# Kernel tuning notes

Measured on AMD Instinct MI355X. Metric: run time of the kernel, lower is better.

The kernel has to match this reference:

```python
import jax, jax.numpy as jnp
import numpy as np

N, E = 50000, 800000          # nodes, edges (avg degree 16)
D_IN, D_H, D_OUT = 128, 128, 64
BN_EPS = 1e-5


def setup_inputs() -> dict:
    key = jax.random.key(0)
    ks = jax.random.split(key, 8)
    g = lambda k, shp, s: jax.random.normal(k, shp, jnp.float32) * s
    return {
        "x": jax.random.normal(ks[0], (N, D_IN), jnp.float32),
        "edge_index": jax.random.randint(ks[1], (2, E), 0, N),
        # SAGEConv layer 1: lin_l (neighbors, with bias), lin_r (root, no bias)
        "Wl1": g(ks[2], (D_IN, D_H), 0.05),
        "Wr1": g(ks[3], (D_IN, D_H), 0.05),
        "b1": jnp.zeros((D_H,), jnp.float32),
        # BatchNorm1d(hidden)
        "gamma": jnp.ones((D_H,), jnp.float32),
        "beta": jnp.zeros((D_H,), jnp.float32),
        # SAGEConv layer 2
        "Wl2": g(ks[4], (D_H, D_OUT), 0.05),
        "Wr2": g(ks[5], (D_H, D_OUT), 0.05),
        "b2": jnp.zeros((D_OUT,), jnp.float32),
    }


def _sage_conv(x, src, dst, Wl, Wr, b):
    """PyG SAGEConv (mean aggr): lin_l(mean_{j in N(i)} x_j) + lin_r(x_i)."""
    n = x.shape[0]
    agg = jax.ops.segment_sum(x[src], dst, num_segments=n)            # [N, d]
    cnt = jax.ops.segment_sum(jnp.ones((src.shape[0],), x.dtype), dst,
                              num_segments=n)                          # [N]
    agg = agg / jnp.maximum(cnt, 1.0)[:, None]                         # mean, 0 for isolated
    return agg @ Wl + x @ Wr + b


def _batch_norm(x, gamma, beta):
    """Training-mode BatchNorm1d: batch stats over the node axis, biased var."""
    mu = jnp.mean(x, axis=0)
    var = jnp.var(x, axis=0)
    return gamma * (x - mu) * jax.lax.rsqrt(var + BN_EPS) + beta


def reference(x, edge_index, Wl1, Wr1, b1, gamma, beta, Wl2, Wr2, b2):
    src, dst = edge_index[0], edge_index[1]
    h = _sage_conv(x, src, dst, Wl1, Wr1, b1)
    h = jax.nn.relu(_batch_norm(h, gamma, beta))
    # dropout is identity in eval / deterministic reference
    return _sage_conv(h, src, dst, Wl2, Wr2, b2)
```

## Files before the change

kernel.cpp:

```cpp
#include <hip/hip_runtime.h>
#include <hip/hip_bf16.h>

#define DIN   128
#define DH    128
#define DOUTC 64
#define BN_EPS 1e-5f

typedef __attribute__((ext_vector_type(8))) short bf16x8;
typedef __attribute__((ext_vector_type(4))) float f32x4;

__device__ inline unsigned short f2bf(float f) {
    __hip_bfloat16 b = __float2bfloat16(f);
    return *reinterpret_cast<unsigned short*>(&b);
}
__device__ inline float bf2f(unsigned short u) {
    return __uint_as_float(((unsigned int)u) << 16);
}

__device__ inline void block_excl_scan_256(const int* __restrict__ arr,
                                           int* __restrict__ excl,
                                           int* __restrict__ wsum, int tid)
{
    int lane = tid & 63, w = tid >> 6;
    int v = arr[tid];
    int inc = v;
    #pragma unroll
    for (int off = 1; off < 64; off <<= 1) {
        int t = __shfl_up(inc, off, 64);
        if (lane >= off) inc += t;
    }
    if (lane == 63) wsum[w] = inc;
    __syncthreads();
    if (tid == 0) {
        int s = 0;
        #pragma unroll
        for (int i = 0; i < 4; ++i) { int t = wsum[i]; wsum[i] = s; s += t; }
    }
    __syncthreads();
    excl[tid] = inc - v + wsum[w];
    __syncthreads();
}

__global__ __launch_bounds__(256) void cvt_bf16_kernel(
    const float* __restrict__ src, unsigned short* __restrict__ dst, int total8)
{
    int i = blockIdx.x * 256 + threadIdx.x;
    if (i >= total8) return;
    float4 a = ((const float4*)src)[2 * i];
    float4 b = ((const float4*)src)[2 * i + 1];
    unsigned short t[8];
    t[0]=f2bf(a.x); t[1]=f2bf(a.y); t[2]=f2bf(a.z); t[3]=f2bf(a.w);
    t[4]=f2bf(b.x); t[5]=f2bf(b.y); t[6]=f2bf(b.z); t[7]=f2bf(b.w);
    *(uint4*)(dst + (size_t)i * 8) = *(uint4*)t;
}

__global__ __launch_bounds__(256) void pack_all_kernel(
    const float* __restrict__ Wl1, const float* __restrict__ Wr1,
    const float* __restrict__ Wl2, const float* __restrict__ Wr2,
    unsigned short* __restrict__ W1p, unsigned short* __restrict__ W2p)
{
    int region = blockIdx.x >> 6;
    int idx = (blockIdx.x & 63) * 256 + threadIdx.x;
    int k = idx >> 7, c = idx & 127;
    int d = ((k >> 5) * 8 + (c >> 4)) * 512 + ((k >> 3) & 3) * 128 + (c & 15) * 8 + (k & 7);
    if (region == 0) {
        W1p[d] = f2bf(Wl1[idx]);
    } else if (region == 1) {
        W1p[128 * 128 + d] = f2bf(Wr1[idx]);
    } else {
        float v = (c < 64) ? Wl2[k * 64 + c] : Wr2[k * 64 + (c - 64)];
        W2p[d] = f2bf(v);
    }
}

__global__ __launch_bounds__(256) void bin_coarse(
    const int* __restrict__ ei, int* __restrict__ cursor,
    unsigned int* __restrict__ coarse, int E, int nb, int cap)
{
    __shared__ int hist[256], lstart[256], gbase[256], wsum[4];
    __shared__ unsigned int staged[4096];
    const int tid = threadIdx.x;
    const int chunkBase = blockIdx.x * 4096;

    hist[tid] = 0;
    __syncthreads();

    unsigned int rec[16]; int pos[16]; int bb[16];
    #pragma unroll
    for (int i = 0; i < 16; ++i) {
        int e = chunkBase + i * 256 + tid;
        if (e < E) {
            int s = ei[e], d = ei[E + e];
            rec[i] = ((unsigned int)d << 16) | (unsigned int)s;
            bb[i]  = d >> 8;
            pos[i] = atomicAdd(&hist[bb[i]], 1);
        } else bb[i] = -1;
    }
    __syncthreads();

    block_excl_scan_256(hist, lstart, wsum, tid);

    if (tid < nb) {
        int c = hist[tid];
        gbase[tid] = c ? atomicAdd(&cursor[tid], c) : 0;
    }
    __syncthreads();

    #pragma unroll
    for (int i = 0; i < 16; ++i)
        if (bb[i] >= 0) staged[lstart[bb[i]] + pos[i]] = rec[i];
    __syncthreads();

    int total = min(4096, E - chunkBase);
    for (int i = tid; i < total; i += 256) {
        unsigned int r = staged[i];
        int b   = (int)(r >> 24);
        int gp  = gbase[b] + (i - lstart[b]);
        if (gp < cap) coarse[(size_t)b * cap + gp] = r;
    }
}

__global__ __launch_bounds__(256) void bin_fine(
    const int* __restrict__ cursor, const unsigned int* __restrict__ coarse,
    unsigned short* __restrict__ sorted, int* __restrict__ deg,
    int* __restrict__ row_start, int n, int cap)
{
    __shared__ int hist[256], pstart[256], cur2[256], wsum[4];
    const int b = blockIdx.x, tid = threadIdx.x;
    const int cnt = min(cursor[b], cap);
    const unsigned int* src = coarse + (size_t)b * cap;

    hist[tid] = 0;
    __syncthreads();

    int nIter = (cnt + 255) >> 8;
    for (int i = 0; i < nIter; ++i) {
        int idx = i * 256 + tid;
        if (idx < cnt) atomicAdd(&hist[(src[idx] >> 16) & 255], 1);
    }
    __syncthreads();

    block_excl_scan_256(hist, pstart, wsum, tid);
    cur2[tid] = pstart[tid];
    __syncthreads();

    for (int i = 0; i < nIter; ++i) {
        int idx = i * 256 + tid;
        if (idx < cnt) {
            unsigned int r = src[idx];
            int dl = (r >> 16) & 255;
            int p  = atomicAdd(&cur2[dl], 1);
            sorted[(size_t)b * cap + p] = (unsigned short)(r & 0xFFFFu);
        }
    }

    int node = b * 256 + tid;
    if (node < n) {
        deg[node]       = hist[tid];
        row_start[node] = b * cap + pstart[tid];
    }
}

__global__ __launch_bounds__(256) void agg_gather128(
    const int* __restrict__ row_start, const int* __restrict__ deg,
    const unsigned short* __restrict__ sorted, const unsigned short* __restrict__ xb,
    unsigned short* __restrict__ aggb, int n)
{
    int wave = (blockIdx.x * 256 + threadIdx.x) >> 6;
    int lane = threadIdx.x & 63;
    if (wave >= n) return;
    int sub  = lane & 15;
    int quad = lane >> 4;
    int base = row_start[wave];
    int d    = deg[wave];
    float acc[8];
    #pragma unroll
    for (int j = 0; j < 8; ++j) acc[j] = 0.f;

    for (int k0 = 0; k0 < d; k0 += 64) {
        int idx = k0 + lane;
        int mys = (idx < d) ? (int)sorted[base + idx] : 0;
        int kmax = min(64, d - k0);
        int kq   = kmax & ~3;
        for (int k = 0; k < kq; k += 4) {
            int s = __shfl(mys, k + quad, 64);
            uint4 raw = ((const uint4*)(xb + (size_t)s * DIN))[sub];
            const unsigned short* u = (const unsigned short*)&raw;
            #pragma unroll
            for (int j = 0; j < 8; ++j) acc[j] += bf2f(u[j]);
        }
        int rem = kmax - kq;
        if (rem) {
            int srcl = kq + quad;
            if (srcl >= kmax) srcl = kmax - 1;
            int s = __shfl(mys, srcl, 64);
            if (quad < rem) {
                uint4 raw = ((const uint4*)(xb + (size_t)s * DIN))[sub];
                const unsigned short* u = (const unsigned short*)&raw;
                #pragma unroll
                for (int j = 0; j < 8; ++j) acc[j] += bf2f(u[j]);
            }
        }
    }
    #pragma unroll
    for (int j = 0; j < 8; ++j) {
        acc[j] += __shfl_xor(acc[j], 32, 64);
        acc[j] += __shfl_xor(acc[j], 16, 64);
    }
    if (quad == 0) {
        float inv = 1.0f / fmaxf((float)d, 1.0f);
        unsigned short t[8];
        #pragma unroll
        for (int j = 0; j < 8; ++j) t[j] = f2bf(acc[j] * inv);
        *(uint4*)(aggb + (size_t)wave * DIN + sub * 8) = *(uint4*)t;
    }
}

__global__ __launch_bounds__(256) void agg_gather64_add(
    const int* __restrict__ row_start, const int* __restrict__ deg,
    const unsigned short* __restrict__ sorted, const unsigned short* __restrict__ P,
    float* __restrict__ out, int n)
{
    int wave = (blockIdx.x * 256 + threadIdx.x) >> 6;
    int lane = threadIdx.x & 63;
    if (wave >= n) return;
    int sub = lane & 7;
    int oct = lane >> 3;
    int base = row_start[wave];
    int d    = deg[wave];
    float acc[8];
    #pragma unroll
    for (int j = 0; j < 8; ++j) acc[j] = 0.f;

    for (int k0 = 0; k0 < d; k0 += 64) {
        int idx = k0 + lane;
        int mys = (idx < d) ? (int)sorted[base + idx] : 0;
        int kmax = min(64, d - k0);
        int ko   = kmax & ~7;
        for (int k = 0; k < ko; k += 8) {
            int s = __shfl(mys, k + oct, 64);
            uint4 raw = ((const uint4*)(P + (size_t)s * DOUTC))[sub];
            const unsigned short* u = (const unsigned short*)&raw;
            #pragma unroll
            for (int j = 0; j < 8; ++j) acc[j] += bf2f(u[j]);
        }
        int rem = kmax - ko;
        if (rem) {
            int srcl = ko + oct;
            if (srcl >= kmax) srcl = kmax - 1;
            int s = __shfl(mys, srcl, 64);
            if (oct < rem) {
                uint4 raw = ((const uint4*)(P + (size_t)s * DOUTC))[sub];
                const unsigned short* u = (const unsigned short*)&raw;
                #pragma unroll
                for (int j = 0; j < 8; ++j) acc[j] += bf2f(u[j]);
            }
        }
    }
    #pragma unroll
    for (int j = 0; j < 8; ++j) {
        acc[j] += __shfl_xor(acc[j], 32, 64);
        acc[j] += __shfl_xor(acc[j], 16, 64);
        acc[j] += __shfl_xor(acc[j],  8, 64);
    }
    if (oct == 0) {
        float inv = 1.0f / fmaxf((float)d, 1.0f);
        float* op = out + (size_t)wave * DOUTC + sub * 8;
        float4 c0 = *(float4*)op;
        float4 c1 = *((float4*)op + 1);
        c0.x += acc[0] * inv; c0.y += acc[1] * inv;
        c0.z += acc[2] * inv; c0.w += acc[3] * inv;
        c1.x += acc[4] * inv; c1.y += acc[5] * inv;
        c1.z += acc[6] * inv; c1.w += acc[7] * inv;
        *(float4*)op = c0;
        *((float4*)op + 1) = c1;
    }
}

__global__ __launch_bounds__(256) void gemm1_mfma(
    const unsigned short* __restrict__ aggb, const unsigned short* __restrict__ xb,
    const unsigned short* __restrict__ W1p, const float* __restrict__ bias,
    float* __restrict__ h,
    float* __restrict__ bn_sum, float* __restrict__ bn_sumsq, int n)
{
    __shared__ union {
        unsigned short A[64][136];
        float red[2][4][128];
    } sm;

    const int block_row = blockIdx.x * 64;
    const int tid  = threadIdx.x;
    const int wave = tid >> 6;
    const int lane = tid & 63;
    const int q    = lane >> 4;
    const int m16  = lane & 15;

    f32x4 acc[8];
    #pragma unroll
    for (int nt = 0; nt < 8; ++nt) acc[nt] = (f32x4){0.f, 0.f, 0.f, 0.f};

    #pragma unroll
    for (int phase = 0; phase < 2; ++phase) {
        const unsigned short* src = phase ? xb : aggb;
        #pragma unroll
        for (int i = 0; i < 4; ++i) {
            int idx = tid + i * 256;
            int r   = idx >> 4;
            int c16 = idx & 15;
            int g   = block_row + r;
            uint4 v = {0u, 0u, 0u, 0u};
            if (g < n) v = ((const uint4*)(src + (size_t)g * DIN))[c16];
            *(uint4*)&sm.A[r][c16 * 8] = v;
        }
        __syncthreads();

        #pragma unroll
        for (int ks = 0; ks < 4; ++ks) {
            bf16x8 a = *(const bf16x8*)&sm.A[wave * 16 + m16][ks * 32 + q * 8];
            const unsigned short* wp = W1p + (size_t)(phase * 4 + ks) * 8 * 512;
            #pragma unroll
            for (int nt = 0; nt < 8; ++nt) {
                bf16x8 b = *(const bf16x8*)(wp + nt * 512 + lane * 8);
                acc[nt] = __builtin_amdgcn_mfma_f32_16x16x32_bf16(a, b, acc[nt], 0, 0, 0);
            }
        }
        __syncthreads();
    }

    float psum[8], psq[8];
    #pragma unroll
    for (int nt = 0; nt < 8; ++nt) {
        int col = nt * 16 + m16;
        float bv = bias[col];
        float s = 0.f, ssq = 0.f;
        #pragma unroll
        for (int reg = 0; reg < 4; ++reg) {
            int g = block_row + wave * 16 + q * 4 + reg;
            float v = acc[nt][reg] + bv;
            if (g < n) {
                h[(size_t)g * DH + col] = v;
                s += v; ssq += v * v;
            }
        }
        psum[nt] = s; psq[nt] = ssq;
    }
    #pragma unroll
    for (int nt = 0; nt < 8; ++nt) {
        psum[nt] += __shfl_xor(psum[nt], 16, 64);
        psum[nt] += __shfl_xor(psum[nt], 32, 64);
        psq[nt]  += __shfl_xor(psq[nt], 16, 64);
        psq[nt]  += __shfl_xor(psq[nt], 32, 64);
    }
    if (lane < 16) {
        #pragma unroll
        for (int nt = 0; nt < 8; ++nt) {
            sm.red[0][wave][nt * 16 + lane] = psum[nt];
            sm.red[1][wave][nt * 16 + lane] = psq[nt];
        }
    }
    __syncthreads();
    if (tid < 128) {
        float s = sm.red[0][0][tid] + sm.red[0][1][tid] +
                  sm.red[0][2][tid] + sm.red[0][3][tid];
        float ssq = sm.red[1][0][tid] + sm.red[1][1][tid] +
                    sm.red[1][2][tid] + sm.red[1][3][tid];
        atomicAdd(&bn_sum[tid], s);
        atomicAdd(&bn_sumsq[tid], ssq);
    }
}

__global__ void bn_finalize_kernel(
    const float* __restrict__ bn_sum, const float* __restrict__ bn_sumsq,
    const float* __restrict__ gamma, const float* __restrict__ beta,
    float* __restrict__ scale, float* __restrict__ shift, int n_nodes)
{
    int c = threadIdx.x;
    if (c >= DH) return;
    float invN = 1.0f / (float)n_nodes;
    float mu  = bn_sum[c] * invN;
    float var = bn_sumsq[c] * invN - mu * mu;
    float sc  = gamma[c] * rsqrtf(var + BN_EPS);
    scale[c] = sc;
    shift[c] = beta[c] - mu * sc;
}

__global__ __launch_bounds__(256) void gemm2p_mfma(
    const float* __restrict__ h,
    const float* __restrict__ scale, const float* __restrict__ shift,
    const unsigned short* __restrict__ W2p, const float* __restrict__ bias,
    unsigned short* __restrict__ P, float* __restrict__ out, int n)
{
    __shared__ unsigned short A[64][136];

    const int block_row = blockIdx.x * 64;
    const int tid  = threadIdx.x;
    const int wave = tid >> 6;
    const int lane = tid & 63;
    const int q    = lane >> 4;
    const int m16  = lane & 15;

    #pragma unroll
    for (int i = 0; i < 8; ++i) {
        int idx = tid + i * 256;
        int r   = idx >> 5;
        int c4  = idx & 31;
        int g   = block_row + r;
        unsigned short t[4] = {0, 0, 0, 0};
        if (g < n) {
            float4 raw = ((const float4*)(h + (size_t)g * DH))[c4];
            float4 sc = ((const float4*)scale)[c4];
            float4 sh = ((const float4*)shift)[c4];
            t[0] = f2bf(fmaxf(raw.x * sc.x + sh.x, 0.f));
            t[1] = f2bf(fmaxf(raw.y * sc.y + sh.y, 0.f));
            t[2] = f2bf(fmaxf(raw.z * sc.z + sh.z, 0.f));
            t[3] = f2bf(fmaxf(raw.w * sc.w + sh.w, 0.f));
        }
        *(uint2*)&A[r][c4 * 4] = *(uint2*)t;
    }
    __syncthreads();

    f32x4 acc[8];
    #pragma unroll
    for (int nt = 0; nt < 8; ++nt) acc[nt] = (f32x4){0.f, 0.f, 0.f, 0.f};

    #pragma unroll
    for (int ks = 0; ks < 4; ++ks) {
        bf16x8 a = *(const bf16x8*)&A[wave * 16 + m16][ks * 32 + q * 8];
        const unsigned short* wp = W2p + (size_t)ks * 8 * 512;
        #pragma unroll
        for (int nt = 0; nt < 8; ++nt) {
            bf16x8 b = *(const bf16x8*)(wp + nt * 512 + lane * 8);
            acc[nt] = __builtin_amdgcn_mfma_f32_16x16x32_bf16(a, b, acc[nt], 0, 0, 0);
        }
    }

    #pragma unroll
    for (int nt = 0; nt < 4; ++nt) {
        int col = nt * 16 + m16;
        #pragma unroll
        for (int reg = 0; reg < 4; ++reg) {
            int g = block_row + wave * 16 + q * 4 + reg;
            if (g < n) P[(size_t)g * DOUTC + col] = f2bf(acc[nt][reg]);
        }
    }
    #pragma unroll
    for (int nt = 4; nt < 8; ++nt) {
        int col = (nt - 4) * 16 + m16;
        float bv = bias[col];
        #pragma unroll
        for (int reg = 0; reg < 4; ++reg) {
            int g = block_row + wave * 16 + q * 4 + reg;
            if (g < n) out[(size_t)g * DOUTC + col] = acc[nt][reg] + bv;
        }
    }
}

extern "C" void kernel_launch(void* const* d_in, const int* in_sizes, int n_in,
                              void* d_out, int out_size, void* d_ws, size_t ws_size,
                              hipStream_t stream)
{
    const float* x     = (const float*)d_in[0];
    const int*   ei    = (const int*)  d_in[1];
    const float* Wl1   = (const float*)d_in[2];
    const float* Wr1   = (const float*)d_in[3];
    const float* b1    = (const float*)d_in[4];
    const float* gamma = (const float*)d_in[5];
    const float* beta  = (const float*)d_in[6];
    const float* Wl2   = (const float*)d_in[7];
    const float* Wr2   = (const float*)d_in[8];
    const float* b2    = (const float*)d_in[9];
    float*       out   = (float*)d_out;

    const int N = in_sizes[0] / DIN;
    const int E = in_sizes[1] / 2;

    const int NB  = (N + 255) >> 8;
    int cap = (E / NB) * 3 / 2 + 256;
    cap = (cap + 255) & ~255;

    float* h        = (float*)d_ws;
    float* bn_sum   = h + (size_t)N * DH;
    float* bn_sumsq = bn_sum + DH;
    float* scale    = bn_sumsq + DH;
    float* shift    = scale + DH;
    int* cursor     = (int*)(shift + DH);
    int* deg        = cursor + 256;
    int* row_start  = deg + N;
    unsigned int* coarse   = (unsigned int*)(row_start + N);
    unsigned short* sorted = (unsigned short*)(coarse + (size_t)NB * cap);
    unsigned short* aggb   = sorted + (size_t)NB * cap;
    unsigned short* xb     = aggb + (size_t)N * DIN;
    unsigned short* P      = xb + (size_t)N * DIN;
    unsigned short* W1p    = P + (size_t)N * DOUTC;
    unsigned short* W2p    = W1p + 256 * 128;

    hipMemsetAsync(bn_sum, 0, (4 * DH + 256) * sizeof(float), stream);

    dim3 blk(256);
    const int binA_blocks = (E + 4095) / 4096;
    const int wave_blocks = (N + 3) / 4;
    const int gemm_blocks = (N + 63) / 64;
    const int cvt_blocks  = ((size_t)N * DIN / 8 + 255) / 256;

    cvt_bf16_kernel<<<cvt_blocks, blk, 0, stream>>>(x, xb, N * DIN / 8);
    pack_all_kernel<<<192, blk, 0, stream>>>(Wl1, Wr1, Wl2, Wr2, W1p, W2p);

    bin_coarse<<<binA_blocks, blk, 0, stream>>>(ei, cursor, coarse, E, NB, cap);
    bin_fine<<<NB, blk, 0, stream>>>(cursor, coarse, sorted, deg, row_start, N, cap);

    agg_gather128<<<wave_blocks, blk, 0, stream>>>(row_start, deg, sorted,
                                                   xb, aggb, N);
    gemm1_mfma<<<gemm_blocks, blk, 0, stream>>>(aggb, xb, W1p, b1, h,
                                                bn_sum, bn_sumsq, N);
    bn_finalize_kernel<<<1, 128, 0, stream>>>(bn_sum, bn_sumsq, gamma, beta,
                                              scale, shift, N);

    gemm2p_mfma<<<gemm_blocks, blk, 0, stream>>>(h, scale, shift, W2p, b2,
                                                 P, out, N);
    agg_gather64_add<<<wave_blocks, blk, 0, stream>>>(row_start, deg, sorted,
                                                      P, out, N);
}
```

Baseline: 228.0 us.

## Gather FP8 node features, store hidden as bf16, fold BN finalize and fuse prep kernels

Adds an FP8 (e4m3) copy of x, and layer-1 neighbor aggregation now gathers those FP8 rows instead of bf16, halving gather bytes. The hidden activation h is stored as bf16 instead of fp32. The BatchNorm finalize kernel is folded into gemm2's prologue, and the x-convert and weight-pack kernels are merged into one launch. This cuts memory traffic and launch count, at the cost of extra FP8 quantization error in the aggregated features and bf16 rounding of h.

Result: faster. 221.3 us (-2.9%).

```diff
diff --git a/kernel.cpp b/kernel.cpp
--- a/kernel.cpp
+++ b/kernel.cpp
@@ -1,5 +1,6 @@
 #include <hip/hip_runtime.h>
 #include <hip/hip_bf16.h>
+#include <hip/hip_fp8.h>
 
 #define DIN   128
 #define DH    128
@@ -8,6 +9,16 @@
 
 typedef __attribute__((ext_vector_type(8))) short bf16x8;
 typedef __attribute__((ext_vector_type(4))) float f32x4;
+typedef __attribute__((ext_vector_type(2))) float f32x2;
+
+#ifndef __has_builtin
+#define __has_builtin(x) 0
+#endif
+#if __has_builtin(__builtin_amdgcn_cvt_pk_f32_fp8) && __has_builtin(__builtin_amdgcn_cvt_pk_fp8_f32)
+#define HW_FP8 1
+#else
+#define HW_FP8 0
+#endif
 
 __device__ inline unsigned short f2bf(float f) {
     __hip_bfloat16 b = __float2bfloat16(f);
@@ -17,6 +28,31 @@
     return __uint_as_float(((unsigned int)u) << 16);
 }
 
+__device__ inline void fp8x4_to_f32(unsigned int w, float* o) {
+#if HW_FP8
+    f32x2 lo = __builtin_amdgcn_cvt_pk_f32_fp8((int)w, false);
+    f32x2 hi = __builtin_amdgcn_cvt_pk_f32_fp8((int)w, true);
+    o[0] = lo.x; o[1] = lo.y; o[2] = hi.x; o[3] = hi.y;
+#else
+    #pragma unroll
+    for (int c = 0; c < 4; ++c) {
+        __hip_fp8_e4m3 q; q.__x = (__hip_fp8_storage_t)((w >> (8 * c)) & 0xFF);
+        o[c] = (float)q;
+    }
+#endif
+}
+__device__ inline unsigned int f32x4_to_fp8(float a, float b, float c, float d) {
+#if HW_FP8
+    int p = __builtin_amdgcn_cvt_pk_fp8_f32(a, b, 0, false);
+    p = __builtin_amdgcn_cvt_pk_fp8_f32(c, d, p, true);
+    return (unsigned int)p;
+#else
+    __hip_fp8_e4m3 qa(a), qb(b), qc(c), qd(d);
+    return (unsigned int)qa.__x | ((unsigned int)qb.__x << 8) |
+           ((unsigned int)qc.__x << 16) | ((unsigned int)qd.__x << 24);
+#endif
+}
+
 __device__ inline void block_excl_scan_256(const int* __restrict__ arr,
                                            int* __restrict__ excl,
                                            int* __restrict__ wsum, int tid)
@@ -41,35 +77,41 @@
     __syncthreads();
 }
 
-__global__ __launch_bounds__(256) void cvt_bf16_kernel(
-    const float* __restrict__ src, unsigned short* __restrict__ dst, int total8)
-{
-    int i = blockIdx.x * 256 + threadIdx.x;
-    if (i >= total8) return;
-    float4 a = ((const float4*)src)[2 * i];
-    float4 b = ((const float4*)src)[2 * i + 1];
-    unsigned short t[8];
-    t[0]=f2bf(a.x); t[1]=f2bf(a.y); t[2]=f2bf(a.z); t[3]=f2bf(a.w);
-    t[4]=f2bf(b.x); t[5]=f2bf(b.y); t[6]=f2bf(b.z); t[7]=f2bf(b.w);
-    *(uint4*)(dst + (size_t)i * 8) = *(uint4*)t;
-}
-
-__global__ __launch_bounds__(256) void pack_all_kernel(
+__global__ __launch_bounds__(256) void cvtpack_kernel(
+    const float* __restrict__ x, unsigned short* __restrict__ xb,
+    unsigned char* __restrict__ xq,
     const float* __restrict__ Wl1, const float* __restrict__ Wr1,
     const float* __restrict__ Wl2, const float* __restrict__ Wr2,
-    unsigned short* __restrict__ W1p, unsigned short* __restrict__ W2p)
-{
-    int region = blockIdx.x >> 6;
-    int idx = (blockIdx.x & 63) * 256 + threadIdx.x;
-    int k = idx >> 7, c = idx & 127;
-    int d = ((k >> 5) * 8 + (c >> 4)) * 512 + ((k >> 3) & 3) * 128 + (c & 15) * 8 + (k & 7);
-    if (region == 0) {
-        W1p[d] = f2bf(Wl1[idx]);
-    } else if (region == 1) {
-        W1p[128 * 128 + d] = f2bf(Wr1[idx]);
+    unsigned short* __restrict__ W1p, unsigned short* __restrict__ W2p,
+    int total8, int cvt_blocks)
+{
+    int b = blockIdx.x;
+    if (b < cvt_blocks) {
+        int i = b * 256 + threadIdx.x;
+        if (i >= total8) return;
+        float4 a = ((const float4*)x)[2 * i];
+        float4 c = ((const float4*)x)[2 * i + 1];
+        unsigned short t[8];
+        t[0]=f2bf(a.x); t[1]=f2bf(a.y); t[2]=f2bf(a.z); t[3]=f2bf(a.w);
+        t[4]=f2bf(c.x); t[5]=f2bf(c.y); t[6]=f2bf(c.z); t[7]=f2bf(c.w);
+        *(uint4*)(xb + (size_t)i * 8) = *(uint4*)t;
+        uint2 pk;
+        pk.x = f32x4_to_fp8(a.x, a.y, a.z, a.w);
+        pk.y = f32x4_to_fp8(c.x, c.y, c.z, c.w);
+        *(uint2*)(xq + (size_t)i * 8) = pk;
     } else {
-        float v = (c < 64) ? Wl2[k * 64 + c] : Wr2[k * 64 + (c - 64)];
-        W2p[d] = f2bf(v);
+        int region = (b - cvt_blocks) >> 6;
+        int idx = ((b - cvt_blocks) & 63) * 256 + threadIdx.x;
+        int k = idx >> 7, c = idx & 127;
+        int d = ((k >> 5) * 8 + (c >> 4)) * 512 + ((k >> 3) & 3) * 128 + (c & 15) * 8 + (k & 7);
+        if (region == 0) {
+            W1p[d] = f2bf(Wl1[idx]);
+        } else if (region == 1) {
+            W1p[128 * 128 + d] = f2bf(Wr1[idx]);
+        } else {
+            float v = (c < 64) ? Wl2[k * 64 + c] : Wr2[k * 64 + (c - 64)];
+            W2p[d] = f2bf(v);
+        }
     }
 }
 
@@ -163,56 +205,69 @@
 
 __global__ __launch_bounds__(256) void agg_gather128(
     const int* __restrict__ row_start, const int* __restrict__ deg,
-    const unsigned short* __restrict__ sorted, const unsigned short* __restrict__ xb,
+    const unsigned short* __restrict__ sorted, const unsigned char* __restrict__ xq,
     unsigned short* __restrict__ aggb, int n)
 {
     int wave = (blockIdx.x * 256 + threadIdx.x) >> 6;
     int lane = threadIdx.x & 63;
     if (wave >= n) return;
-    int sub  = lane & 15;
-    int quad = lane >> 4;
+    int sub = lane & 7;
+    int oct = lane >> 3;
     int base = row_start[wave];
     int d    = deg[wave];
-    float acc[8];
-    #pragma unroll
-    for (int j = 0; j < 8; ++j) acc[j] = 0.f;
+    float acc[16];
+    #pragma unroll
+    for (int j = 0; j < 16; ++j) acc[j] = 0.f;
 
     for (int k0 = 0; k0 < d; k0 += 64) {
         int idx = k0 + lane;
         int mys = (idx < d) ? (int)sorted[base + idx] : 0;
         int kmax = min(64, d - k0);
-        int kq   = kmax & ~3;
-        for (int k = 0; k < kq; k += 4) {
-            int s = __shfl(mys, k + quad, 64);
-            uint4 raw = ((const uint4*)(xb + (size_t)s * DIN))[sub];
-            const unsigned short* u = (const unsigned short*)&raw;
+        int ko   = kmax & ~7;
+        for (int k = 0; k < ko; k += 8) {
+            int s = __shfl(mys, k + oct, 64);
+            uint4 raw = ((const uint4*)(xq + (size_t)s * DIN))[sub];
+            const unsigned int* w = (const unsigned int*)&raw;
             #pragma unroll
-            for (int j = 0; j < 8; ++j) acc[j] += bf2f(u[j]);
-        }
-        int rem = kmax - kq;
+            for (int c = 0; c < 4; ++c) {
+                float o4[4];
+                fp8x4_to_f32(w[c], o4);
+                acc[c*4+0] += o4[0]; acc[c*4+1] += o4[1];
+                acc[c*4+2] += o4[2]; acc[c*4+3] += o4[3];
+            }
+        }
+        int rem = kmax - ko;
         if (rem) {
-            int srcl = kq + quad;
+            int srcl = ko + oct;
             if (srcl >= kmax) srcl = kmax - 1;
             int s = __shfl(mys, srcl, 64);
-            if (quad < rem) {
-                uint4 raw = ((const uint4*)(xb + (size_t)s * DIN))[sub];
-                const unsigned short* u = (const unsigned short*)&raw;
+            if (oct < rem) {
+                uint4 raw = ((const uint4*)(xq + (size_t)s * DIN))[sub];
+                const unsigned int* w = (const unsigned int*)&raw;
                 #pragma unroll
-                for (int j = 0; j < 8; ++j) acc[j] += bf2f(u[j]);
+                for (int c = 0; c < 4; ++c) {
+                    float o4[4];
+                    fp8x4_to_f32(w[c], o4);
+                    acc[c*4+0] += o4[0]; acc[c*4+1] += o4[1];
+                    acc[c*4+2] += o4[2]; acc[c*4+3] += o4[3];
+                }
             }
         }
     }
     #pragma unroll
-    for (int j = 0; j < 8; ++j) {
+    for (int j = 0; j < 16; ++j) {
         acc[j] += __shfl_xor(acc[j], 32, 64);
         acc[j] += __shfl_xor(acc[j], 16, 64);
-    }
-    if (quad == 0) {
+        acc[j] += __shfl_xor(acc[j],  8, 64);
+    }
+    if (oct == 0) {
         float inv = 1.0f / fmaxf((float)d, 1.0f);
-        unsigned short t[8];
-        #pragma unroll
-        for (int j = 0; j < 8; ++j) t[j] = f2bf(acc[j] * inv);
-        *(uint4*)(aggb + (size_t)wave * DIN + sub * 8) = *(uint4*)t;
+        unsigned short t[16];
+        #pragma unroll
+        for (int j = 0; j < 16; ++j) t[j] = f2bf(acc[j] * inv);
+        unsigned short* op = aggb + (size_t)wave * DIN + sub * 16;
+        *(uint4*)op = ((uint4*)t)[0];
+        *(uint4*)(op + 8) = ((uint4*)t)[1];
     }
 }
 
@@ -280,7 +335,7 @@
 __global__ __launch_bounds__(256) void gemm1_mfma(
     const unsigned short* __restrict__ aggb, const unsigned short* __restrict__ xb,
     const unsigned short* __restrict__ W1p, const float* __restrict__ bias,
-    float* __restrict__ h,
+    unsigned short* __restrict__ hb,
     float* __restrict__ bn_sum, float* __restrict__ bn_sumsq, int n)
 {
     __shared__ union {
@@ -338,7 +393,7 @@
             int g = block_row + wave * 16 + q * 4 + reg;
             float v = acc[nt][reg] + bv;
             if (g < n) {
-                h[(size_t)g * DH + col] = v;
+                hb[(size_t)g * DH + col] = f2bf(v);
                 s += v; ssq += v * v;
             }
         }
@@ -369,28 +424,15 @@
     }
 }
 
-__global__ void bn_finalize_kernel(
+__global__ __launch_bounds__(256) void gemm2p_mfma(
+    const unsigned short* __restrict__ hb,
     const float* __restrict__ bn_sum, const float* __restrict__ bn_sumsq,
     const float* __restrict__ gamma, const float* __restrict__ beta,
-    float* __restrict__ scale, float* __restrict__ shift, int n_nodes)
-{
-    int c = threadIdx.x;
-    if (c >= DH) return;
-    float invN = 1.0f / (float)n_nodes;
-    float mu  = bn_sum[c] * invN;
-    float var = bn_sumsq[c] * invN - mu * mu;
-    float sc  = gamma[c] * rsqrtf(var + BN_EPS);
-    scale[c] = sc;
-    shift[c] = beta[c] - mu * sc;
-}
-
-__global__ __launch_bounds__(256) void gemm2p_mfma(
-    const float* __restrict__ h,
-    const float* __restrict__ scale, const float* __restrict__ shift,
     const unsigned short* __restrict__ W2p, const float* __restrict__ bias,
     unsigned short* __restrict__ P, float* __restrict__ out, int n)
 {
     __shared__ unsigned short A[64][136];
+    __shared__ float s_scale[128], s_shift[128];
 
     const int block_row = blockIdx.x * 64;
     const int tid  = threadIdx.x;
@@ -399,23 +441,34 @@
     const int q    = lane >> 4;
     const int m16  = lane & 15;
 
-    #pragma unroll
-    for (int i = 0; i < 8; ++i) {
+    if (tid < 128) {
+        float invN = 1.0f / (float)n;
+        float mu  = bn_sum[tid] * invN;
+        float var = bn_sumsq[tid] * invN - mu * mu;
+        float sc  = gamma[tid] * rsqrtf(var + BN_EPS);
+        s_scale[tid] = sc;
+        s_shift[tid] = beta[tid] - mu * sc;
+    }
+    __syncthreads();
+
+    #pragma unroll
+    for (int i = 0; i < 4; ++i) {
         int idx = tid + i * 256;
-        int r   = idx >> 5;
-        int c4  = idx & 31;
+        int r   = idx >> 4;
+        int c16 = idx & 15;
         int g   = block_row + r;
-        unsigned short t[4] = {0, 0, 0, 0};
+        unsigned short t[8] = {0,0,0,0,0,0,0,0};
         if (g < n) {
-            float4 raw = ((const float4*)(h + (size_t)g * DH))[c4];
-            float4 sc = ((const float4*)scale)[c4];
-            float4 sh = ((const float4*)shift)[c4];
-            t[0] = f2bf(fmaxf(raw.x * sc.x + sh.x, 0.f));
-            t[1] = f2bf(fmaxf(raw.y * sc.y + sh.y, 0.f));
-            t[2] = f2bf(fmaxf(raw.z * sc.z + sh.z, 0.f));
-            t[3] = f2bf(fmaxf(raw.w * sc.w + sh.w, 0.f));
-        }
-        *(uint2*)&A[r][c4 * 4] = *(uint2*)t;
+            uint4 raw = ((const uint4*)(hb + (size_t)g * DH))[c16];
+            const unsigned short* u = (const unsigned short*)&raw;
+            #pragma unroll
+            for (int j = 0; j < 8; ++j) {
+                int col = c16 * 8 + j;
+                float v = bf2f(u[j]) * s_scale[col] + s_shift[col];
+                t[j] = f2bf(fmaxf(v, 0.f));
+            }
+        }
+        *(uint4*)&A[r][c16 * 8] = *(uint4*)t;
     }
     __syncthreads();
 
@@ -478,44 +531,42 @@
     int cap = (E / NB) * 3 / 2 + 256;
     cap = (cap + 255) & ~255;
 
-    float* h        = (float*)d_ws;
-    float* bn_sum   = h + (size_t)N * DH;
+    float* bn_sum   = (float*)d_ws;
     float* bn_sumsq = bn_sum + DH;
-    float* scale    = bn_sumsq + DH;
-    float* shift    = scale + DH;
-    int* cursor     = (int*)(shift + DH);
+    int* cursor     = (int*)(bn_sumsq + DH);
     int* deg        = cursor + 256;
     int* row_start  = deg + N;
     unsigned int* coarse   = (unsigned int*)(row_start + N);
     unsigned short* sorted = (unsigned short*)(coarse + (size_t)NB * cap);
-    unsigned short* aggb   = sorted + (size_t)NB * cap;
+    unsigned short* hb     = sorted + (size_t)NB * cap;
+    unsigned short* aggb   = hb + (size_t)N * DH;
     unsigned short* xb     = aggb + (size_t)N * DIN;
     unsigned short* P      = xb + (size_t)N * DIN;
     unsigned short* W1p    = P + (size_t)N * DOUTC;
     unsigned short* W2p    = W1p + 256 * 128;
-
-    hipMemsetAsync(bn_sum, 0, (4 * DH + 256) * sizeof(float), stream);
+    unsigned char*  xq     = (unsigned char*)(W2p + 128 * 128);
+
+    hipMemsetAsync(bn_sum, 0, (2 * DH + 256) * sizeof(float), stream);
 
     dim3 blk(256);
     const int binA_blocks = (E + 4095) / 4096;
     const int wave_blocks = (N + 3) / 4;
     const int gemm_blocks = (N + 63) / 64;
-    const int cvt_blocks  = ((size_t)N * DIN / 8 + 255) / 256;
-
-    cvt_bf16_kernel<<<cvt_blocks, blk, 0, stream>>>(x, xb, N * DIN / 8);
-    pack_all_kernel<<<192, blk, 0, stream>>>(Wl1, Wr1, Wl2, Wr2, W1p, W2p);
+    const int cvt_blocks  = (N * DIN / 8 + 255) / 256;
+
+    cvtpack_kernel<<<cvt_blocks + 192, blk, 0, stream>>>(
+        x, xb, xq, Wl1, Wr1, Wl2, Wr2, W1p, W2p, N * DIN / 8, cvt_blocks);
 
     bin_coarse<<<binA_blocks, blk, 0, stream>>>(ei, cursor, coarse, E, NB, cap);
     bin_fine<<<NB, blk, 0, stream>>>(cursor, coarse, sorted, deg, row_start, N, cap);
 
     agg_gather128<<<wave_blocks, blk, 0, stream>>>(row_start, deg, sorted,
-                                                   xb, aggb, N);
-    gemm1_mfma<<<gemm_blocks, blk, 0, stream>>>(aggb, xb, W1p, b1, h,
+                                                   xq, aggb, N);
+    gemm1_mfma<<<gemm_blocks, blk, 0, stream>>>(aggb, xb, W1p, b1, hb,
                                                 bn_sum, bn_sumsq, N);
-    bn_finalize_kernel<<<1, 128, 0, stream>>>(bn_sum, bn_sumsq, gamma, beta,
-                                              scale, shift, N);
-
-    gemm2p_mfma<<<gemm_blocks, blk, 0, stream>>>(h, scale, shift, W2p, b2,
+
+    gemm2p_mfma<<<gemm_blocks, blk, 0, stream>>>(hb, bn_sum, bn_sumsq,
+                                                 gamma, beta, W2p, b2,
                                                  P, out, N);
     agg_gather64_add<<<wave_blocks, blk, 0, stream>>>(row_start, deg, sorted,
                                                       P, out, N);
```
